# Optimization experiments

Measured on AMD Instinct MI355X. Metric: run time of the kernel, lower is better.

Reference implementation:

```python
import jax, jax.numpy as jnp
import numpy as np

N_HEAD = 16
N_KV_HEAD = 8
HEAD_DIM = 128
N_EMBED = 2048
EPS = 1.1920929e-07  # torch default eps for fp32 rms_norm


def _apply_rotary_emb(x, cos, sin):
    # x: (B, T, H, D); cos/sin: (1, T, 1, D//2)  (nanochat-style half rotation)
    d = x.shape[-1] // 2
    x1, x2 = x[..., :d], x[..., d:]
    y1 = x1 * cos + x2 * sin
    y2 = -x1 * sin + x2 * cos
    return jnp.concatenate([y1, y2], axis=-1).astype(x.dtype)


def _rms_norm(x):
    return x * jax.lax.rsqrt(jnp.mean(jnp.square(x), axis=-1, keepdims=True) + EPS)


def setup_inputs() -> dict:
    key = jax.random.key(0)
    ks = jax.random.split(key, 5)
    B, T = 2, 2048
    kv_dim = N_KV_HEAD * HEAD_DIM
    x = jax.random.normal(ks[0], (B, T, N_EMBED), dtype=jnp.float32)
    w_attn = jax.random.normal(ks[1], (N_EMBED + 2 * kv_dim, N_EMBED), dtype=jnp.float32) * 0.02
    w_proj = jax.random.normal(ks[2], (N_EMBED, N_EMBED), dtype=jnp.float32) * 0.02
    # realistic RoPE tables
    half = HEAD_DIM // 2
    inv_freq = 1.0 / (10000.0 ** (jnp.arange(half, dtype=jnp.float32) / half))
    freqs = jnp.arange(T, dtype=jnp.float32)[:, None] * inv_freq[None, :]  # (T, half)
    cos = jnp.cos(freqs)[None, :, None, :]
    sin = jnp.sin(freqs)[None, :, None, :]
    return {"x": x, "w_attn": w_attn, "w_proj": w_proj, "cos": cos, "sin": sin}


def reference(x, w_attn, w_proj, cos, sin):
    B, T, C = x.shape
    kv_dim = N_KV_HEAD * HEAD_DIM
    qkv = jnp.einsum('btc,oc->bto', x, w_attn)  # (B, T, C + 2*kv_dim)
    q = qkv[..., :C].reshape(B, T, N_HEAD, HEAD_DIM)
    k = qkv[..., C:C + kv_dim].reshape(B, T, N_KV_HEAD, HEAD_DIM)
    v = qkv[..., C + kv_dim:].reshape(B, T, N_KV_HEAD, HEAD_DIM)
    q = _rms_norm(_apply_rotary_emb(q, cos, sin))
    k = _rms_norm(_apply_rotary_emb(k, cos, sin))
    # GQA: repeat kv heads to match query heads
    rep = N_HEAD // N_KV_HEAD
    k = jnp.repeat(k, rep, axis=2)  # (B, T, n_head, D)
    v = jnp.repeat(v, rep, axis=2)
    scale = 1.0 / jnp.sqrt(jnp.float32(HEAD_DIM))
    scores = jnp.einsum('bqhd,bkhd->bhqk', q, k) * scale  # (B, H, T, T)
    causal = jnp.tril(jnp.ones((T, T), dtype=bool))
    scores = jnp.where(causal[None, None], scores, jnp.finfo(scores.dtype).min)
    attn = jax.nn.softmax(scores, axis=-1)
    y = jnp.einsum('bhqk,bkhd->bqhd', attn, v).reshape(B, T, C)
    return jnp.einsum('btc,oc->bto', y, w_proj)
```

## Files before the change

### kernel.cpp

```cpp
#include <hip/hip_runtime.h>

#define B_ 2
#define T_ 2048
#define NH 16
#define NKV 8
#define HD 128
#define C_ 2048
#define KVD (NKV*HD)
#define QKVD (C_ + 2*KVD)
#define NTOK (B_*T_)

typedef __bf16 bf16_t;
typedef __bf16 bf16x2_t __attribute__((ext_vector_type(2)));
typedef __bf16 bf16x4_t __attribute__((ext_vector_type(4)));
typedef __bf16 bf16x8_t __attribute__((ext_vector_type(8)));
typedef float f32x4_t __attribute__((ext_vector_type(4)));
typedef float f32x16_t __attribute__((ext_vector_type(16)));
typedef int i32x4_t __attribute__((ext_vector_type(4)));

__device__ __forceinline__ f32x4_t mfma16(bf16x8_t a, bf16x8_t b, f32x4_t c) {
  return __builtin_amdgcn_mfma_f32_16x16x32_bf16(a, b, c, 0, 0, 0);
}
__device__ __forceinline__ f32x16_t mfma32(bf16x8_t a, bf16x8_t b, f32x16_t c) {
  return __builtin_amdgcn_mfma_f32_32x32x16_bf16(a, b, c, 0, 0, 0);
}
__device__ __forceinline__ f32x16_t zero16() {
  f32x16_t z;
  #pragma unroll
  for (int i = 0; i < 16; i++) z[i] = 0.f;
  return z;
}
__device__ __forceinline__ int pk2(float a, float b) {
  bf16x2_t t; t[0] = (bf16_t)a; t[1] = (bf16_t)b;
  return __builtin_bit_cast(int, t);
}

#define GLDS16(gp, lp) __builtin_amdgcn_global_load_lds( \
    (const __attribute__((address_space(1))) void*)(gp), \
    (__attribute__((address_space(3))) void*)(lp), 16, 0, 0)

__global__ __launch_bounds__(256) void cvt3_kernel(const float* __restrict__ s0, bf16_t* __restrict__ d0,
                                                   const float* __restrict__ s1, bf16_t* __restrict__ d1,
                                                   const float* __restrict__ s2, bf16_t* __restrict__ d2) {
  int bid = blockIdx.x;
  const float* s; bf16_t* d; int off;
  if (bid < 8192)       { s = s0; d = d0; off = bid; }
  else if (bid < 16384) { s = s1; d = d1; off = bid - 8192; }
  else                  { s = s2; d = d2; off = bid - 16384; }
  int i = (off * 256 + threadIdx.x) * 4;
  const float4 v = *(const float4*)(s + i);
  bf16x4_t o;
  o[0] = (bf16_t)v.x; o[1] = (bf16_t)v.y; o[2] = (bf16_t)v.z; o[3] = (bf16_t)v.w;
  *(bf16x4_t*)(d + i) = o;
}

__global__ void gemm_nt(const bf16_t* __restrict__ A, const bf16_t* __restrict__ Bm,
                        float* __restrict__ Cf, bf16_t* __restrict__ Cb, int M, int N, int K) {
  __shared__ bf16_t As[128*32];
  __shared__ bf16_t Bs[128*32];
  int tid = threadIdx.x;
  int wave = tid >> 6, lane = tid & 63;
  int quad = lane >> 4, l16 = lane & 15;
  int wm = (wave >> 1) * 64, wn = (wave & 1) * 64;
  int bm = blockIdx.y * 128, bn = blockIdx.x * 128;
  int grow = wave * 32 + (lane >> 2);
  int gcol = (lane & 3) * 8;
  const bf16_t* pa = A + (size_t)(bm + grow) * K + gcol;
  const bf16_t* pb = Bm + (size_t)(bn + grow) * K + gcol;
  bf16_t* lA0 = &As[(wave * 32) * 32];
  bf16_t* lA1 = &As[(wave * 32 + 16) * 32];
  bf16_t* lB0 = &Bs[(wave * 32) * 32];
  bf16_t* lB1 = &Bs[(wave * 32 + 16) * 32];
  f32x4_t acc[4][4];
  #pragma unroll
  for (int i = 0; i < 4; i++)
    #pragma unroll
    for (int j = 0; j < 4; j++) acc[i][j] = (f32x4_t){0.f,0.f,0.f,0.f};
  for (int k0 = 0; k0 < K; k0 += 32) {
    __syncthreads();
    GLDS16(pa + k0, lA0);
    GLDS16(pa + (size_t)16 * K + k0, lA1);
    GLDS16(pb + k0, lB0);
    GLDS16(pb + (size_t)16 * K + k0, lB1);
    __syncthreads();
    bf16x8_t af[4], bfr[4];
    #pragma unroll
    for (int i = 0; i < 4; i++) {
      af[i]  = *(const bf16x8_t*)&As[(wm + i*16 + l16)*32 + quad*8];
      bfr[i] = *(const bf16x8_t*)&Bs[(wn + i*16 + l16)*32 + quad*8];
    }
    #pragma unroll
    for (int i = 0; i < 4; i++)
      #pragma unroll
      for (int j = 0; j < 4; j++)
        acc[i][j] = mfma16(af[i], bfr[j], acc[i][j]);
  }
  if (Cb) {
    #pragma unroll
    for (int i = 0; i < 4; i++)
      #pragma unroll
      for (int j = 0; j < 4; j++) {
        int row0 = bm + wm + i*16 + quad*4;
        int col  = bn + wn + j*16 + l16;
        #pragma unroll
        for (int r = 0; r < 4; r++)
          Cb[(size_t)(row0 + r) * N + col] = (bf16_t)acc[i][j][r];
      }
  } else {
    #pragma unroll
    for (int i = 0; i < 4; i++)
      #pragma unroll
      for (int j = 0; j < 4; j++) {
        int row0 = bm + wm + i*16 + quad*4;
        int col  = bn + wn + j*16 + l16;
        #pragma unroll
        for (int r = 0; r < 4; r++)
          Cf[(size_t)(row0 + r) * N + col] = acc[i][j][r];
      }
  }
}

__global__ __launch_bounds__(256) void rope_norm_kernel(const bf16_t* __restrict__ qkv,
    const float* __restrict__ cosb, const float* __restrict__ sinb,
    bf16_t* __restrict__ qb, bf16_t* __restrict__ kb) {
  int token = blockIdx.y;
  int slot = blockIdx.x * 4 + (threadIdx.x >> 6);
  int lane = threadIdx.x & 63;
  int b = token >> 11, s = token & 2047;
  const bf16_t* row = qkv + (size_t)token * QKVD;
  int base_in = (slot < 16) ? slot * HD : C_ + (slot - 16) * HD;
  float x1 = (float)row[base_in + lane];
  float x2 = (float)row[base_in + 64 + lane];
  float c = cosb[s*64 + lane], sn = sinb[s*64 + lane];
  float y1 = x1*c + x2*sn;
  float y2 = x2*c - x1*sn;
  float ss = y1*y1 + y2*y2;
  ss += __shfl_xor(ss, 1);  ss += __shfl_xor(ss, 2);  ss += __shfl_xor(ss, 4);
  ss += __shfl_xor(ss, 8);  ss += __shfl_xor(ss, 16); ss += __shfl_xor(ss, 32);
  float r = rsqrtf(ss * (1.0f/128.0f) + 1.1920929e-07f);
  bf16_t* dst;
  if (slot < 16) {
    r *= 0.08838834764831845f * 1.4426950408889634f;
    dst = qb + ((size_t)(b*NH + slot) * T_ + s) * HD;
  } else {
    dst = kb + ((size_t)(b*NKV + (slot-16)) * T_ + s) * HD;
  }
  dst[lane]      = (bf16_t)(y1 * r);
  dst[lane + 64] = (bf16_t)(y2 * r);
}

__global__ __launch_bounds__(256) void transpose_v(const bf16_t* __restrict__ qkv,
                                                   bf16_t* __restrict__ vt) {
  __shared__ bf16_t TT[64*136];
  int bk = blockIdx.y;
  int b = bk >> 3, kv = bk & 7;
  int s0 = blockIdx.x * 64;
  int tid = threadIdx.x;
  int row = tid >> 2, c0 = (tid & 3) * 32;
  const bf16_t* src = qkv + (size_t)(b*T_ + s0 + row) * QKVD + C_ + KVD + kv*HD + c0;
  #pragma unroll
  for (int s4 = 0; s4 < 4; s4++)
    *(bf16x8_t*)&TT[row*136 + c0 + s4*8] = *(const bf16x8_t*)(src + s4*8);
  __syncthreads();
  #pragma unroll
  for (int s2 = 0; s2 < 2; s2++) {
    int d = (tid >> 2) + s2*64;
    #pragma unroll
    for (int s = 0; s < 2; s++) {
      int g = (tid & 3) * 8 + s*32;
      bf16x8_t pk;
      #pragma unroll
      for (int e = 0; e < 8; e++) pk[e] = TT[(g + e)*136 + d];
      *(bf16x8_t*)(vt + ((size_t)bk * HD + d) * T_ + s0 + g) = pk;
    }
  }
}

__global__ __launch_bounds__(512, 1) void attn_kernel(const bf16_t* __restrict__ qb,
    const bf16_t* __restrict__ kb, const bf16_t* __restrict__ vt, bf16_t* __restrict__ yb) {
  __shared__ __align__(16) bf16_t Ks[2][2][64*136];
  __shared__ __align__(16) bf16_t Vs[2][2][128*72];
  int L = blockIdx.x;
  int bh = L & 31;
  int qt = 15 - (L >> 5);
  int b = bh >> 4, h = bh & 15, kvh = h >> 1;
  int tid = threadIdx.x;
  int wv = tid >> 6;
  int g  = wv >> 2;
  int sq = wv & 3;
  int lane = tid & 63;
  int l32 = lane & 31, half = lane >> 5;
  int t256 = tid & 255;
  const bf16_t* Qp = qb + (size_t)bh * T_ * HD;
  const bf16_t* Kp = kb + (size_t)(b*NKV + kvh) * T_ * HD;
  const bf16_t* Vt = vt + (size_t)(b*NKV + kvh) * HD * T_;

  int krow = t256 >> 2, kcb = (t256 & 3) * 32;
  int vd = t256 >> 1,  vcb = (t256 & 1) * 32;

  int h0 = qt + 1;
  int kt0 = g * h0;

  int qrow = qt*128 + sq*32 + l32;
  bf16x8_t qf[8];
  #pragma unroll
  for (int kc = 0; kc < 8; kc++)
    qf[kc] = *(const bf16x8_t*)(Qp + (size_t)qrow * HD + kc*16 + half*8);

  float mrow = -1e30f, lrow = 0.f;
  f32x16_t o[4];
  #pragma unroll
  for (int mb = 0; mb < 4; mb++) o[mb] = zero16();

  bf16x8_t kreg[4], vreg[4];
  {
    const bf16_t* srck = Kp + (size_t)(kt0*64 + krow) * HD + kcb;
    const bf16_t* srcv = Vt + (size_t)vd * T_ + kt0*64 + vcb;
    #pragma unroll
    for (int s2 = 0; s2 < 4; s2++) { kreg[s2] = *(const bf16x8_t*)(srck + s2*8);
                                     vreg[s2] = *(const bf16x8_t*)(srcv + s2*8); }
  }
  #pragma unroll
  for (int s2 = 0; s2 < 4; s2++) { *(bf16x8_t*)&Ks[g][0][krow*136 + kcb + s2*8] = kreg[s2];
                                   *(bf16x8_t*)&Vs[g][0][vd*72   + vcb + s2*8] = vreg[s2]; }

  for (int t = 0; t < h0; t++) {
    __syncthreads();
    int cur = t & 1;
    if (t + 1 < h0) {
      int k1 = (kt0 + t + 1) * 64;
      const bf16_t* srck = Kp + (size_t)(k1 + krow) * HD + kcb;
      const bf16_t* srcv = Vt + (size_t)vd * T_ + k1 + vcb;
      #pragma unroll
      for (int s2 = 0; s2 < 4; s2++) { kreg[s2] = *(const bf16x8_t*)(srck + s2*8);
                                       vreg[s2] = *(const bf16x8_t*)(srcv + s2*8); }
    }
    int k0 = (kt0 + t) * 64;
    f32x16_t sacc[2];
    sacc[0] = zero16(); sacc[1] = zero16();
    #pragma unroll
    for (int kc = 0; kc < 8; kc++)
      #pragma unroll
      for (int mb = 0; mb < 2; mb++) {
        bf16x8_t kf = *(const bf16x8_t*)&Ks[g][cur][(mb*32 + l32)*136 + kc*16 + half*8];
        sacc[mb] = mfma32(kf, qf[kc], sacc[mb]);
      }
    if (k0 + 63 > qt*128 + sq*32) {
      #pragma unroll
      for (int mb = 0; mb < 2; mb++)
        #pragma unroll
        for (int r = 0; r < 16; r++) {
          int key = k0 + mb*32 + (r&3) + 8*(r>>2) + 4*half;
          if (key > qrow) sacc[mb][r] = -1e30f;
        }
    }
    float mx = -1e30f;
    #pragma unroll
    for (int mb = 0; mb < 2; mb++)
      #pragma unroll
      for (int r = 0; r < 16; r++) mx = fmaxf(mx, sacc[mb][r]);
    mx = fmaxf(mx, __shfl_xor(mx, 32));
    float mnew = fmaxf(mrow, mx);
    float alpha = exp2f(mrow - mnew);
    mrow = mnew;
    float rs = 0.f;
    #pragma unroll
    for (int mb = 0; mb < 2; mb++)
      #pragma unroll
      for (int r = 0; r < 16; r++) {
        float p = exp2f(sacc[mb][r] - mnew);
        sacc[mb][r] = p;
        rs += p;
      }
    rs += __shfl_xor(rs, 32);
    lrow = lrow * alpha + rs;
    #pragma unroll
    for (int mb = 0; mb < 4; mb++) o[mb] = o[mb] * alpha;
    int P2[2][4][2];
    #pragma unroll
    for (int mb = 0; mb < 2; mb++)
      #pragma unroll
      for (int gg = 0; gg < 4; gg++) {
        P2[mb][gg][0] = pk2(sacc[mb][4*gg+0], sacc[mb][4*gg+1]);
        P2[mb][gg][1] = pk2(sacc[mb][4*gg+2], sacc[mb][4*gg+3]);
      }
    #pragma unroll
    for (int kc = 0; kc < 4; kc++) {
      int mb = kc >> 1, c = kc & 1;
      int o0 = half ? P2[mb][2*c+1][0] : P2[mb][2*c][0];
      int o1 = half ? P2[mb][2*c+1][1] : P2[mb][2*c][1];
      int s0 = half ? P2[mb][2*c][0]   : P2[mb][2*c+1][0];
      int s1 = half ? P2[mb][2*c][1]   : P2[mb][2*c+1][1];
      int r0 = __shfl_xor(s0, 32);
      int r1 = __shfl_xor(s1, 32);
      i32x4_t wvv;
      wvv[0] = half ? r0 : o0;
      wvv[1] = half ? r1 : o1;
      wvv[2] = half ? o0 : r0;
      wvv[3] = half ? o1 : r1;
      bf16x8_t pf = __builtin_bit_cast(bf16x8_t, wvv);
      #pragma unroll
      for (int mbd = 0; mbd < 4; mbd++) {
        bf16x8_t vf = *(const bf16x8_t*)&Vs[g][cur][(mbd*32 + l32)*72 + kc*16 + half*8];
        o[mbd] = mfma32(vf, pf, o[mbd]);
      }
    }
    if (t + 1 < h0) {
      #pragma unroll
      for (int s2 = 0; s2 < 4; s2++) { *(bf16x8_t*)&Ks[g][1-cur][krow*136 + kcb + s2*8] = kreg[s2];
                                       *(bf16x8_t*)&Vs[g][1-cur][vd*72   + vcb + s2*8] = vreg[s2]; }
    }
  }
  __syncthreads();
  float* MG = (float*)Vs;
  int mbase = (sq*64 + lane) * 66;
  if (g == 1) {
    #pragma unroll
    for (int mb = 0; mb < 4; mb++)
      #pragma unroll
      for (int r = 0; r < 16; r++) MG[mbase + mb*16 + r] = o[mb][r];
    MG[mbase + 64] = mrow;
    MG[mbase + 65] = lrow;
  }
  __syncthreads();
  if (g == 0) {
    float m1 = MG[mbase + 64], l1v = MG[mbase + 65];
    float mm = fmaxf(mrow, m1);
    float a0 = exp2f(mrow - mm), a1 = exp2f(m1 - mm);
    float invl = 1.0f / (lrow * a0 + l1v * a1);
    a0 *= invl; a1 *= invl;
    bf16_t* OL = &((bf16_t*)Ks)[sq * 4352];
    #pragma unroll
    for (int mb = 0; mb < 4; mb++)
      #pragma unroll
      for (int rr = 0; rr < 4; rr++) {
        bf16x4_t pk;
        #pragma unroll
        for (int jj = 0; jj < 4; jj++)
          pk[jj] = (bf16_t)(o[mb][rr*4+jj] * a0 + MG[mbase + mb*16 + rr*4 + jj] * a1);
        *(bf16x4_t*)&OL[l32*136 + mb*32 + rr*8 + half*4] = pk;
      }
    int tok = qt*128 + sq*32 + l32;
    bf16_t* dst = yb + ((size_t)(b*T_ + tok) * NH + h) * HD + half*64;
    #pragma unroll
    for (int jj = 0; jj < 8; jj++)
      *(bf16x8_t*)(dst + jj*8) = *(const bf16x8_t*)&OL[l32*136 + half*64 + jj*8];
  }
}

extern "C" void kernel_launch(void* const* d_in, const int* in_sizes, int n_in,
                              void* d_out, int out_size, void* d_ws, size_t ws_size,
                              hipStream_t stream) {
  const float* x      = (const float*)d_in[0];
  const float* w_attn = (const float*)d_in[1];
  const float* w_proj = (const float*)d_in[2];
  const float* cosb   = (const float*)d_in[3];
  const float* sinb   = (const float*)d_in[4];
  float* out = (float*)d_out;

  bf16_t* xb   = (bf16_t*)d_ws;
  bf16_t* wab  = xb + 8388608;
  bf16_t* wpb  = wab + 8388608;
  bf16_t* qkvb = wpb + 4194304;
  bf16_t* qb   = qkvb + 16777216;
  bf16_t* kb   = qb + 8388608;
  bf16_t* vt   = kb + 4194304;
  bf16_t* yb   = vt + 4194304;

  cvt3_kernel<<<20480, 256, 0, stream>>>(x, xb, w_attn, wab, w_proj, wpb);

  gemm_nt<<<dim3(32, 32), 256, 0, stream>>>(xb, wab, nullptr, qkvb, NTOK, QKVD, C_);

  rope_norm_kernel<<<dim3(6, 4096), 256, 0, stream>>>(qkvb, cosb, sinb, qb, kb);
  transpose_v<<<dim3(32, 16), 256, 0, stream>>>(qkvb, vt);

  attn_kernel<<<512, 512, 0, stream>>>(qb, kb, vt, yb);

  gemm_nt<<<dim3(16, 32), 256, 0, stream>>>(yb, wpb, out, nullptr, NTOK, C_, C_);
}
```

Before: 335.8 us.

## Rewrite GEMM with larger tiles, double-buffered LDS, XOR swizzle and grid remap

Replaces the 128x128, K=32 single-buffered GEMM with a templated 512-thread kernel using 256-wide N tiles, K=64 steps, and double-buffered LDS so global-to-LDS loads of the next tile overlap the MFMAs on the current one. LDS columns are XOR-swizzled to avoid bank conflicts, and block indices are remapped so neighbouring workgroups spread across the grid, aiming at better L2 reuse. Larger tiles raise per-thread register use and LDS footprint and shrink the grid (256 workgroups per GEMM), so occupancy and load balance across CUs may suffer.

```diff
diff --git a/kernel.cpp b/kernel.cpp
--- a/kernel.cpp
+++ b/kernel.cpp
@@ -54,70 +54,95 @@
   *(bf16x4_t*)(d + i) = o;
 }
 
-__global__ void gemm_nt(const bf16_t* __restrict__ A, const bf16_t* __restrict__ Bm,
-                        float* __restrict__ Cf, bf16_t* __restrict__ Cb, int M, int N, int K) {
-  __shared__ bf16_t As[128*32];
-  __shared__ bf16_t Bs[128*32];
+template<int BM>
+__global__ __launch_bounds__(512, 1) void gemm_nt2(const bf16_t* __restrict__ A,
+                                                   const bf16_t* __restrict__ Bm,
+                                                   float* __restrict__ Cf, bf16_t* __restrict__ Cb,
+                                                   int M, int N, int K) {
+  constexpr int MR = BM / 32;
+  constexpr int RA = BM / 64;
+  __shared__ __align__(16) bf16_t As[2][BM * 64];
+  __shared__ __align__(16) bf16_t Bs[2][256 * 64];
   int tid = threadIdx.x;
   int wave = tid >> 6, lane = tid & 63;
   int quad = lane >> 4, l16 = lane & 15;
-  int wm = (wave >> 1) * 64, wn = (wave & 1) * 64;
-  int bm = blockIdx.y * 128, bn = blockIdx.x * 128;
-  int grow = wave * 32 + (lane >> 2);
-  int gcol = (lane & 3) * 8;
-  const bf16_t* pa = A + (size_t)(bm + grow) * K + gcol;
-  const bf16_t* pb = Bm + (size_t)(bn + grow) * K + gcol;
-  bf16_t* lA0 = &As[(wave * 32) * 32];
-  bf16_t* lA1 = &As[(wave * 32 + 16) * 32];
-  bf16_t* lB0 = &Bs[(wave * 32) * 32];
-  bf16_t* lB1 = &Bs[(wave * 32 + 16) * 32];
-  f32x4_t acc[4][4];
-  #pragma unroll
-  for (int i = 0; i < 4; i++)
-    #pragma unroll
-    for (int j = 0; j < 4; j++) acc[i][j] = (f32x4_t){0.f,0.f,0.f,0.f};
-  for (int k0 = 0; k0 < K; k0 += 32) {
+  int wm = wave >> 2, wn = wave & 3;
+  int gx = gridDim.x;
+  int nwg = gx * gridDim.y;
+  int flat = blockIdx.y * gx + blockIdx.x;
+  int swz = (flat & 7) * (nwg >> 3) + (flat >> 3);
+  int bm = (swz / gx) * BM, bn = (swz % gx) * 256;
+  int scol = (((tid & 7) ^ ((tid >> 3) & 7))) * 8;
+  const bf16_t* pa = A + (size_t)(bm + (tid >> 3)) * K + scol;
+  const bf16_t* pb = Bm + (size_t)(bn + (tid >> 3)) * K + scol;
+  int ldsrow = (tid >> 3) * 64;
+
+  f32x4_t acc[MR][4];
+  #pragma unroll
+  for (int i = 0; i < MR; i++)
+    #pragma unroll
+    for (int j = 0; j < 4; j++) acc[i][j] = (f32x4_t){0.f, 0.f, 0.f, 0.f};
+
+  int nt = K >> 6;
+  #pragma unroll
+  for (int r = 0; r < RA; r++) GLDS16(pa + (size_t)(r * 64) * K, &As[0][(r * 64 + wave * 8) * 64]);
+  #pragma unroll
+  for (int r = 0; r < 4; r++)  GLDS16(pb + (size_t)(r * 64) * K, &Bs[0][(r * 64 + wave * 8) * 64]);
+  __syncthreads();
+
+  for (int t = 0; t < nt; t++) {
+    int cur = t & 1;
+    if (t + 1 < nt) {
+      int k1 = (t + 1) * 64;
+      #pragma unroll
+      for (int r = 0; r < RA; r++) GLDS16(pa + (size_t)(r * 64) * K + k1, &As[1 - cur][(r * 64 + wave * 8) * 64]);
+      #pragma unroll
+      for (int r = 0; r < 4; r++)  GLDS16(pb + (size_t)(r * 64) * K + k1, &Bs[1 - cur][(r * 64 + wave * 8) * 64]);
+    }
+    bf16x8_t bfr[4][2];
+    #pragma unroll
+    for (int ni = 0; ni < 4; ni++)
+      #pragma unroll
+      for (int kh = 0; kh < 2; kh++) {
+        int blk = (kh * 4 + quad) ^ (l16 & 7);
+        bfr[ni][kh] = *(const bf16x8_t*)&Bs[cur][(wn * 64 + ni * 16 + l16) * 64 + blk * 8];
+      }
+    #pragma unroll
+    for (int g = 0; g < MR / 2; g++) {
+      bf16x8_t af[2][2];
+      #pragma unroll
+      for (int i = 0; i < 2; i++)
+        #pragma unroll
+        for (int kh = 0; kh < 2; kh++) {
+          int blk = (kh * 4 + quad) ^ (l16 & 7);
+          af[i][kh] = *(const bf16x8_t*)&As[cur][(wm * (BM / 2) + (g * 2 + i) * 16 + l16) * 64 + blk * 8];
+        }
+      #pragma unroll
+      for (int kh = 0; kh < 2; kh++)
+        #pragma unroll
+        for (int i = 0; i < 2; i++)
+          #pragma unroll
+          for (int ni = 0; ni < 4; ni++)
+            acc[g * 2 + i][ni] = mfma16(af[i][kh], bfr[ni][kh], acc[g * 2 + i][ni]);
+    }
     __syncthreads();
-    GLDS16(pa + k0, lA0);
-    GLDS16(pa + (size_t)16 * K + k0, lA1);
-    GLDS16(pb + k0, lB0);
-    GLDS16(pb + (size_t)16 * K + k0, lB1);
-    __syncthreads();
-    bf16x8_t af[4], bfr[4];
-    #pragma unroll
-    for (int i = 0; i < 4; i++) {
-      af[i]  = *(const bf16x8_t*)&As[(wm + i*16 + l16)*32 + quad*8];
-      bfr[i] = *(const bf16x8_t*)&Bs[(wn + i*16 + l16)*32 + quad*8];
-    }
-    #pragma unroll
-    for (int i = 0; i < 4; i++)
-      #pragma unroll
-      for (int j = 0; j < 4; j++)
-        acc[i][j] = mfma16(af[i], bfr[j], acc[i][j]);
-  }
-  if (Cb) {
-    #pragma unroll
-    for (int i = 0; i < 4; i++)
-      #pragma unroll
-      for (int j = 0; j < 4; j++) {
-        int row0 = bm + wm + i*16 + quad*4;
-        int col  = bn + wn + j*16 + l16;
+  }
+  #pragma unroll
+  for (int mi = 0; mi < MR; mi++)
+    #pragma unroll
+    for (int ni = 0; ni < 4; ni++) {
+      int row0 = bm + wm * (BM / 2) + mi * 16 + quad * 4;
+      int col  = bn + wn * 64 + ni * 16 + l16;
+      if (Cb) {
         #pragma unroll
         for (int r = 0; r < 4; r++)
-          Cb[(size_t)(row0 + r) * N + col] = (bf16_t)acc[i][j][r];
-      }
-  } else {
-    #pragma unroll
-    for (int i = 0; i < 4; i++)
-      #pragma unroll
-      for (int j = 0; j < 4; j++) {
-        int row0 = bm + wm + i*16 + quad*4;
-        int col  = bn + wn + j*16 + l16;
+          Cb[(size_t)(row0 + r) * N + col] = (bf16_t)acc[mi][ni][r];
+      } else {
         #pragma unroll
         for (int r = 0; r < 4; r++)
-          Cf[(size_t)(row0 + r) * N + col] = acc[i][j][r];
-      }
-  }
+          Cf[(size_t)(row0 + r) * N + col] = acc[mi][ni][r];
+      }
+    }
 }
 
 __global__ __launch_bounds__(256) void rope_norm_kernel(const bf16_t* __restrict__ qkv,
@@ -369,12 +394,12 @@
 
   cvt3_kernel<<<20480, 256, 0, stream>>>(x, xb, w_attn, wab, w_proj, wpb);
 
-  gemm_nt<<<dim3(32, 32), 256, 0, stream>>>(xb, wab, nullptr, qkvb, NTOK, QKVD, C_);
+  gemm_nt2<256><<<dim3(16, 16), 512, 0, stream>>>(xb, wab, nullptr, qkvb, NTOK, QKVD, C_);
 
   rope_norm_kernel<<<dim3(6, 4096), 256, 0, stream>>>(qkvb, cosb, sinb, qb, kb);
   transpose_v<<<dim3(32, 16), 256, 0, stream>>>(qkvb, vt);
 
   attn_kernel<<<512, 512, 0, stream>>>(qb, kb, vt, yb);
 
-  gemm_nt<<<dim3(16, 32), 256, 0, stream>>>(yb, wpb, out, nullptr, NTOK, C_, C_);
-}
+  gemm_nt2<128><<<dim3(8, 32), 512, 0, stream>>>(yb, wpb, out, nullptr, NTOK, C_, C_);
+}
```

Measured after the change: 321.7 us. 1.04x faster.
